# Kernel optimization log

Measured on AMD Instinct MI355X. Metric: run time of the kernel, lower is better.

Reference implementation:

```python
import jax, jax.numpy as jnp
import numpy as np

D_MODEL = 1024
D_FF = 4 * D_MODEL
NUM_EXPERTS = 8
TOP_K = 2
TOKENS = 4096


def setup_inputs() -> dict:
    key = jax.random.key(0)
    ks = jax.random.split(key, 8)
    s = 0.02
    x = jax.random.normal(ks[0], (TOKENS, D_MODEL), dtype=jnp.float32)
    Wg = jax.random.normal(ks[1], (D_MODEL, NUM_EXPERTS), dtype=jnp.float32) * s
    bg = jnp.zeros((NUM_EXPERTS,), dtype=jnp.float32)
    W1 = jax.random.normal(ks[2], (NUM_EXPERTS, D_MODEL, D_FF), dtype=jnp.float32) * s
    b1 = jnp.zeros((NUM_EXPERTS, D_FF), dtype=jnp.float32)
    W2 = jax.random.normal(ks[3], (NUM_EXPERTS, D_FF, D_MODEL), dtype=jnp.float32) * s
    b2 = jnp.zeros((NUM_EXPERTS, D_MODEL), dtype=jnp.float32)
    return {"x": x, "Wg": Wg, "bg": bg, "W1": W1, "b1": b1, "W2": W2, "b2": b2}


def reference(x, Wg, bg, W1, b1, W2, b2):
    # Gating: softmax over experts, select top-k indices per token.
    gate_scores = jax.nn.softmax(x @ Wg + bg, axis=-1)        # [T, E]
    _, top_k_idx = jax.lax.top_k(gate_scores, TOP_K)          # [T, K]
    # Binary combine mask: 1 where expert selected (top_k indices are distinct).
    # NOTE: original sums selected expert outputs WITHOUT gate weighting.
    mask = jnp.sum(jax.nn.one_hot(top_k_idx, NUM_EXPERTS, dtype=x.dtype), axis=1)  # [T, E]
    out = jnp.zeros_like(x)
    for e in range(NUM_EXPERTS):  # small fixed expert count
        h = jax.nn.relu(x @ W1[e] + b1[e])                    # [T, 4D]
        y = h @ W2[e] + b2[e]                                 # [T, D]
        out = out + mask[:, e:e + 1] * y
    return out
```

## Files before the change

kernel.cpp:

```cpp
#include <hip/hip_runtime.h>
#include <hip/hip_bf16.h>

#define T_TOKENS 4096
#define DM 1024
#define DF 4096
#define NE 8
#define MAXROWS 9216

typedef float f32x4 __attribute__((ext_vector_type(4)));
typedef short bf16x8 __attribute__((ext_vector_type(8)));

__device__ __forceinline__ unsigned short f2bf(float f) {
    union { float f; unsigned int u; } v; v.f = f;
    unsigned int r = v.u + 0x7fffu + ((v.u >> 16) & 1u);
    return (unsigned short)(r >> 16);
}

__device__ __forceinline__ void g2l16(const void* g, void* l) {
    __builtin_amdgcn_global_load_lds(
        (const __attribute__((address_space(1))) void*)g,
        (__attribute__((address_space(3))) void*)l, 16, 0, 0);
}

__global__ __launch_bounds__(256) void gate_kernel(
    const float* __restrict__ x, const float* __restrict__ Wg, const float* __restrict__ bg,
    int* __restrict__ counts, int* __restrict__ topk)
{
    int wave = threadIdx.x >> 6;
    int lane = threadIdx.x & 63;
    int t = blockIdx.x * 4 + wave;
    float acc[NE];
#pragma unroll
    for (int e = 0; e < NE; e++) acc[e] = 0.f;
    const float* xr = x + (size_t)t * DM;
#pragma unroll
    for (int i = 0; i < DM / 64; i++) {
        int d = lane + i * 64;
        float xv = xr[d];
        const float4* wg = (const float4*)(Wg + d * NE);
        float4 w0 = wg[0], w1 = wg[1];
        acc[0] += xv * w0.x; acc[1] += xv * w0.y; acc[2] += xv * w0.z; acc[3] += xv * w0.w;
        acc[4] += xv * w1.x; acc[5] += xv * w1.y; acc[6] += xv * w1.z; acc[7] += xv * w1.w;
    }
#pragma unroll
    for (int e = 0; e < NE; e++) {
#pragma unroll
        for (int off = 32; off > 0; off >>= 1)
            acc[e] += __shfl_down(acc[e], off);
    }
    if (lane == 0) {
        float lg[NE];
#pragma unroll
        for (int e = 0; e < NE; e++) lg[e] = acc[e] + bg[e];
        int b1i = 0; float b1v = lg[0];
        for (int e = 1; e < NE; e++) if (lg[e] > b1v) { b1v = lg[e]; b1i = e; }
        int b2i = -1; float b2v = -1e30f;
        for (int e = 0; e < NE; e++) {
            if (e == b1i) continue;
            if (b2i < 0 || lg[e] > b2v) { b2v = lg[e]; b2i = e; }
        }
        topk[t * 2 + 0] = b1i;
        topk[t * 2 + 1] = b2i;
        atomicAdd(&counts[b1i], 1);
        atomicAdd(&counts[b2i], 1);
    }
}

__global__ __launch_bounds__(256) void scatter_kernel(
    const int* __restrict__ counts, const int* __restrict__ topk,
    int* __restrict__ offsets, int* __restrict__ list)
{
    __shared__ int offs[NE + 1];
    __shared__ int cur[NE];
    if (threadIdx.x == 0) {
        int s = 0;
        for (int e = 0; e < NE; e++) {
            offs[e] = s; offsets[e] = s;
            s += (counts[e] + 127) & ~127;
        }
        offs[NE] = s; offsets[NE] = s;
    }
    if (threadIdx.x < NE) cur[threadIdx.x] = 0;
    __syncthreads();
    for (int i = threadIdx.x; i < T_TOKENS * 2; i += 256) {
        int e = topk[i];
        int pos = atomicAdd(&cur[e], 1);
        list[offs[e] + pos] = i >> 1;
    }
    __syncthreads();
    for (int e = 0; e < NE; e++) {
        int s = offs[e] + counts[e];
        int t = offs[e + 1];
        for (int i = s + threadIdx.x; i < t; i += 256) list[i] = -1;
    }
}

__global__ __launch_bounds__(256) void cvt_x_kernel(
    const float* __restrict__ x, unsigned short* __restrict__ xb)
{
    int i = (blockIdx.x * 256 + threadIdx.x) * 4;
    float4 v = *(const float4*)(x + i);
    unsigned short o[4] = { f2bf(v.x), f2bf(v.y), f2bf(v.z), f2bf(v.w) };
    *(uint2*)(xb + i) = *(const uint2*)o;
}

__global__ __launch_bounds__(256) void tr_cvt_kernel(
    const float* __restrict__ src, unsigned short* __restrict__ dst, int K, int N)
{
    const int e = blockIdx.z;
    src += (size_t)e * K * N;
    dst += (size_t)e * N * K;
    const int n0 = blockIdx.x * 64, k0 = blockIdx.y * 64;
    __shared__ unsigned short tile[64][68];
    const int t = threadIdx.x;
    const int tx = t & 63, ty = t >> 6;
#pragma unroll
    for (int r = 0; r < 16; r++) {
        int k = ty * 16 + r;
        tile[tx][k] = f2bf(src[(size_t)(k0 + k) * N + n0 + tx]);
    }
    __syncthreads();
    const int kx = (t & 15) * 4, ny = t >> 4;
#pragma unroll
    for (int r = 0; r < 4; r++) {
        int n = ny + r * 16;
        *(uint2*)(dst + (size_t)(n0 + n) * K + k0 + kx) = *(const uint2*)&tile[n][kx];
    }
}

__global__ __launch_bounds__(256) void gemm1_kernel(
    const unsigned short* __restrict__ xb, const unsigned short* __restrict__ W1T,
    const float* __restrict__ b1, const int* __restrict__ offsets,
    const int* __restrict__ list, unsigned short* __restrict__ H)
{
    const int total = offsets[NE];
    const int row0 = blockIdx.x * 128;
    if (row0 >= total) return;
    int e = 0;
    while (row0 >= offsets[e + 1]) e++;
    const int n0 = blockIdx.y * 128;

    __shared__ unsigned short Asm[2][4096];
    __shared__ unsigned short Bsm[2][4096];

    const int tid = threadIdx.x;
    const int w = tid >> 6, lane = tid & 63;
    const int quad = lane >> 4, l16 = lane & 15;
    const int wm = w >> 1, wn = w & 1;

    const int sr = lane >> 2;
    const int sc = (((lane & 3) ^ ((sr >> 1) & 3))) * 8;
    const int qx8 = (quad ^ ((l16 >> 1) & 3)) * 8;

    const int ra1 = 32 * w + sr, ra2 = ra1 + 16;
    int t1 = list[row0 + ra1]; if (t1 < 0) t1 = 0;
    int t2 = list[row0 + ra2]; if (t2 < 0) t2 = 0;
    const unsigned short* gA1 = xb + (size_t)t1 * DM + sc;
    const unsigned short* gA2 = xb + (size_t)t2 * DM + sc;
    const unsigned short* Wb = W1T + (size_t)e * DF * DM;
    const unsigned short* gB1 = Wb + (size_t)(n0 + 32 * w + sr) * DM + sc;
    const unsigned short* gB2 = gB1 + (size_t)16 * DM;
    unsigned short* lA1 = &Asm[0][(2 * w) * 512];
    unsigned short* lA2 = &Asm[0][(2 * w + 1) * 512];
    unsigned short* lB1 = &Bsm[0][(2 * w) * 512];
    unsigned short* lB2 = &Bsm[0][(2 * w + 1) * 512];

    f32x4 acc[4][4];
#pragma unroll
    for (int i = 0; i < 4; i++)
#pragma unroll
        for (int j = 0; j < 4; j++) acc[i][j] = (f32x4){0.f, 0.f, 0.f, 0.f};

#define STAGE1(b, kk) do { \
        g2l16(gA1 + (kk), lA1 + (b) * 4096); \
        g2l16(gA2 + (kk), lA2 + (b) * 4096); \
        g2l16(gB1 + (kk), lB1 + (b) * 4096); \
        g2l16(gB2 + (kk), lB2 + (b) * 4096); } while (0)

    STAGE1(0, 0);
    __syncthreads();
#pragma unroll 2
    for (int kk = 0; kk < DM; kk += 32) {
        const int b = (kk >> 5) & 1;
        if (kk + 32 < DM) STAGE1(b ^ 1, kk + 32);
        bf16x8 af[4];
#pragma unroll
        for (int i = 0; i < 4; i++)
            af[i] = *(const bf16x8*)&Asm[b][(wm * 64 + i * 16 + l16) * 32 + qx8];
#pragma unroll
        for (int j = 0; j < 4; j++) {
            bf16x8 bfv = *(const bf16x8*)&Bsm[b][(wn * 64 + j * 16 + l16) * 32 + qx8];
#pragma unroll
            for (int i = 0; i < 4; i++)
                acc[i][j] = __builtin_amdgcn_mfma_f32_16x16x32_bf16(af[i], bfv, acc[i][j], 0, 0, 0);
        }
        __syncthreads();
    }
#undef STAGE1

    const float* bias = b1 + e * DF;
#pragma unroll
    for (int j = 0; j < 4; j++) {
        int n = n0 + wn * 64 + j * 16 + l16;
        float bj = bias[n];
#pragma unroll
        for (int i = 0; i < 4; i++) {
            int row = row0 + wm * 64 + i * 16 + quad * 4;
#pragma unroll
            for (int r = 0; r < 4; r++) {
                float v = acc[i][j][r] + bj;
                v = fmaxf(v, 0.f);
                H[(size_t)(row + r) * DF + n] = f2bf(v);
            }
        }
    }
}

__global__ __launch_bounds__(256) void gemm2_kernel(
    const unsigned short* __restrict__ H, const unsigned short* __restrict__ W2T,
    const float* __restrict__ b2, const int* __restrict__ offsets,
    const int* __restrict__ list, float* __restrict__ out)
{
    const int total = offsets[NE];
    const int row0 = blockIdx.x * 128;
    if (row0 >= total) return;
    int e = 0;
    while (row0 >= offsets[e + 1]) e++;
    const int n0 = blockIdx.y * 128;
    const int kz = blockIdx.z;
    const int k0 = kz * (DF / 2);

    __shared__ unsigned short Asm[2][4096];
    __shared__ unsigned short Bsm[2][4096];

    const int tid = threadIdx.x;
    const int w = tid >> 6, lane = tid & 63;
    const int quad = lane >> 4, l16 = lane & 15;
    const int wm = w >> 1, wn = w & 1;

    const int sr = lane >> 2;
    const int sc = (((lane & 3) ^ ((sr >> 1) & 3))) * 8;
    const int qx8 = (quad ^ ((l16 >> 1) & 3)) * 8;

    const unsigned short* gA1 = H + (size_t)(row0 + 32 * w + sr) * DF + k0 + sc;
    const unsigned short* gA2 = gA1 + (size_t)16 * DF;
    const unsigned short* Wb = W2T + (size_t)e * DM * DF;
    const unsigned short* gB1 = Wb + (size_t)(n0 + 32 * w + sr) * DF + k0 + sc;
    const unsigned short* gB2 = gB1 + (size_t)16 * DF;
    unsigned short* lA1 = &Asm[0][(2 * w) * 512];
    unsigned short* lA2 = &Asm[0][(2 * w + 1) * 512];
    unsigned short* lB1 = &Bsm[0][(2 * w) * 512];
    unsigned short* lB2 = &Bsm[0][(2 * w + 1) * 512];

    f32x4 acc[4][4];
#pragma unroll
    for (int i = 0; i < 4; i++)
#pragma unroll
        for (int j = 0; j < 4; j++) acc[i][j] = (f32x4){0.f, 0.f, 0.f, 0.f};

#define STAGE2(b, kk) do { \
        g2l16(gA1 + (kk), lA1 + (b) * 4096); \
        g2l16(gA2 + (kk), lA2 + (b) * 4096); \
        g2l16(gB1 + (kk), lB1 + (b) * 4096); \
        g2l16(gB2 + (kk), lB2 + (b) * 4096); } while (0)

    STAGE2(0, 0);
    __syncthreads();
#pragma unroll 2
    for (int kk = 0; kk < DF / 2; kk += 32) {
        const int b = (kk >> 5) & 1;
        if (kk + 32 < DF / 2) STAGE2(b ^ 1, kk + 32);
        bf16x8 af[4];
#pragma unroll
        for (int i = 0; i < 4; i++)
            af[i] = *(const bf16x8*)&Asm[b][(wm * 64 + i * 16 + l16) * 32 + qx8];
#pragma unroll
        for (int j = 0; j < 4; j++) {
            bf16x8 bfv = *(const bf16x8*)&Bsm[b][(wn * 64 + j * 16 + l16) * 32 + qx8];
#pragma unroll
            for (int i = 0; i < 4; i++)
                acc[i][j] = __builtin_amdgcn_mfma_f32_16x16x32_bf16(af[i], bfv, acc[i][j], 0, 0, 0);
        }
        __syncthreads();
    }
#undef STAGE2

    const float* bias = b2 + e * DM;
#pragma unroll
    for (int j = 0; j < 4; j++) {
        int n = n0 + wn * 64 + j * 16 + l16;
        float bj = (kz == 0) ? bias[n] : 0.f;
#pragma unroll
        for (int i = 0; i < 4; i++) {
            int row = row0 + wm * 64 + i * 16 + quad * 4;
#pragma unroll
            for (int r = 0; r < 4; r++) {
                int tk = list[row + r];
                if (tk >= 0)
                    atomicAdd(&out[(size_t)tk * DM + n], acc[i][j][r] + bj);
            }
        }
    }
}

extern "C" void kernel_launch(void* const* d_in, const int* in_sizes, int n_in,
                              void* d_out, int out_size, void* d_ws, size_t ws_size,
                              hipStream_t stream)
{
    const float* x  = (const float*)d_in[0];
    const float* Wg = (const float*)d_in[1];
    const float* bg = (const float*)d_in[2];
    const float* W1 = (const float*)d_in[3];
    const float* b1 = (const float*)d_in[4];
    const float* W2 = (const float*)d_in[5];
    const float* b2 = (const float*)d_in[6];
    float* out = (float*)d_out;

    char* ws = (char*)d_ws;
    int* counts  = (int*)(ws + 0);
    int* offsets = (int*)(ws + 64);
    int* topk    = (int*)(ws + 256);
    int* list    = (int*)(ws + 33024);
    unsigned short* xb = (unsigned short*)(ws + (1u << 20));
    unsigned short* WT = (unsigned short*)(ws + (16u << 20));
    unsigned short* Hb = (unsigned short*)(ws + (80u << 20));

    hipMemsetAsync(counts, 0, NE * sizeof(int), stream);
    hipMemsetAsync(d_out, 0, (size_t)out_size * sizeof(float), stream);

    gate_kernel<<<T_TOKENS / 4, 256, 0, stream>>>(x, Wg, bg, counts, topk);
    scatter_kernel<<<1, 256, 0, stream>>>(counts, topk, offsets, list);
    cvt_x_kernel<<<T_TOKENS * DM / 1024, 256, 0, stream>>>(x, xb);

    tr_cvt_kernel<<<dim3(DF / 64, DM / 64, NE), 256, 0, stream>>>(W1, WT, DM, DF);
    gemm1_kernel<<<dim3(MAXROWS / 128, DF / 128), 256, 0, stream>>>(
        xb, WT, b1, offsets, list, Hb);

    tr_cvt_kernel<<<dim3(DM / 64, DF / 64, NE), 256, 0, stream>>>(W2, WT, DF, DM);
    gemm2_kernel<<<dim3(MAXROWS / 128, DM / 128, 2), 256, 0, stream>>>(
        Hb, WT, b2, offsets, list, out);
}
```

Baseline: 716.2 us.

## Triple-buffer LDS pipeline with vmcnt waits; drop split-K in gemm2

Both expert GEMMs move from double-buffered LDS staging with a full __syncthreads per k-step to a three-stage ring. Loads run two tiles ahead, and an explicit s_waitcnt vmcnt(4) plus a raw s_barrier is used in place of draining all outstanding loads. The aim is to hide global-to-LDS latency better. gemm2 also drops its 2-way split-K over DF, which halves the atomicAdd traffic to the output but also halves the grid size and doubles the K loop per block.

```diff
diff --git a/kernel.cpp b/kernel.cpp
--- a/kernel.cpp
+++ b/kernel.cpp
@@ -140,8 +140,8 @@
     while (row0 >= offsets[e + 1]) e++;
     const int n0 = blockIdx.y * 128;
 
-    __shared__ unsigned short Asm[2][4096];
-    __shared__ unsigned short Bsm[2][4096];
+    __shared__ unsigned short Asm[3][4096];
+    __shared__ unsigned short Bsm[3][4096];
 
     const int tid = threadIdx.x;
     const int w = tid >> 6, lane = tid & 63;
@@ -177,12 +177,7 @@
         g2l16(gB1 + (kk), lB1 + (b) * 4096); \
         g2l16(gB2 + (kk), lB2 + (b) * 4096); } while (0)
 
-    STAGE1(0, 0);
-    __syncthreads();
-#pragma unroll 2
-    for (int kk = 0; kk < DM; kk += 32) {
-        const int b = (kk >> 5) & 1;
-        if (kk + 32 < DM) STAGE1(b ^ 1, kk + 32);
+    auto compute = [&](int b) {
         bf16x8 af[4];
 #pragma unroll
         for (int i = 0; i < 4; i++)
@@ -194,8 +189,24 @@
             for (int i = 0; i < 4; i++)
                 acc[i][j] = __builtin_amdgcn_mfma_f32_16x16x32_bf16(af[i], bfv, acc[i][j], 0, 0, 0);
         }
-        __syncthreads();
-    }
+    };
+
+    const int NT = DM / 32;
+    STAGE1(0, 0);
+    STAGE1(1, 32);
+    int bc = 0, bs = 2;
+    for (int t = 0; t < NT - 1; ++t) {
+        asm volatile("s_waitcnt vmcnt(4)" ::: "memory");
+        __builtin_amdgcn_s_barrier();
+        __builtin_amdgcn_sched_barrier(0);
+        if (t + 2 < NT) STAGE1(bs, (t + 2) * 32);
+        compute(bc);
+        bc = (bc == 2) ? 0 : bc + 1;
+        bs = (bs == 2) ? 0 : bs + 1;
+    }
+    asm volatile("s_waitcnt vmcnt(0)" ::: "memory");
+    __builtin_amdgcn_s_barrier();
+    compute(bc);
 #undef STAGE1
 
     const float* bias = b1 + e * DF;
@@ -227,11 +238,9 @@
     int e = 0;
     while (row0 >= offsets[e + 1]) e++;
     const int n0 = blockIdx.y * 128;
-    const int kz = blockIdx.z;
-    const int k0 = kz * (DF / 2);
-
-    __shared__ unsigned short Asm[2][4096];
-    __shared__ unsigned short Bsm[2][4096];
+
+    __shared__ unsigned short Asm[3][4096];
+    __shared__ unsigned short Bsm[3][4096];
 
     const int tid = threadIdx.x;
     const int w = tid >> 6, lane = tid & 63;
@@ -242,10 +251,10 @@
     const int sc = (((lane & 3) ^ ((sr >> 1) & 3))) * 8;
     const int qx8 = (quad ^ ((l16 >> 1) & 3)) * 8;
 
-    const unsigned short* gA1 = H + (size_t)(row0 + 32 * w + sr) * DF + k0 + sc;
+    const unsigned short* gA1 = H + (size_t)(row0 + 32 * w + sr) * DF + sc;
     const unsigned short* gA2 = gA1 + (size_t)16 * DF;
     const unsigned short* Wb = W2T + (size_t)e * DM * DF;
-    const unsigned short* gB1 = Wb + (size_t)(n0 + 32 * w + sr) * DF + k0 + sc;
+    const unsigned short* gB1 = Wb + (size_t)(n0 + 32 * w + sr) * DF + sc;
     const unsigned short* gB2 = gB1 + (size_t)16 * DF;
     unsigned short* lA1 = &Asm[0][(2 * w) * 512];
     unsigned short* lA2 = &Asm[0][(2 * w + 1) * 512];
@@ -264,12 +273,7 @@
         g2l16(gB1 + (kk), lB1 + (b) * 4096); \
         g2l16(gB2 + (kk), lB2 + (b) * 4096); } while (0)
 
-    STAGE2(0, 0);
-    __syncthreads();
-#pragma unroll 2
-    for (int kk = 0; kk < DF / 2; kk += 32) {
-        const int b = (kk >> 5) & 1;
-        if (kk + 32 < DF / 2) STAGE2(b ^ 1, kk + 32);
+    auto compute = [&](int b) {
         bf16x8 af[4];
 #pragma unroll
         for (int i = 0; i < 4; i++)
@@ -281,15 +285,31 @@
             for (int i = 0; i < 4; i++)
                 acc[i][j] = __builtin_amdgcn_mfma_f32_16x16x32_bf16(af[i], bfv, acc[i][j], 0, 0, 0);
         }
-        __syncthreads();
-    }
+    };
+
+    const int NT = DF / 32;
+    STAGE2(0, 0);
+    STAGE2(1, 32);
+    int bc = 0, bs = 2;
+    for (int t = 0; t < NT - 1; ++t) {
+        asm volatile("s_waitcnt vmcnt(4)" ::: "memory");
+        __builtin_amdgcn_s_barrier();
+        __builtin_amdgcn_sched_barrier(0);
+        if (t + 2 < NT) STAGE2(bs, (t + 2) * 32);
+        compute(bc);
+        bc = (bc == 2) ? 0 : bc + 1;
+        bs = (bs == 2) ? 0 : bs + 1;
+    }
+    asm volatile("s_waitcnt vmcnt(0)" ::: "memory");
+    __builtin_amdgcn_s_barrier();
+    compute(bc);
 #undef STAGE2
 
     const float* bias = b2 + e * DM;
 #pragma unroll
     for (int j = 0; j < 4; j++) {
         int n = n0 + wn * 64 + j * 16 + l16;
-        float bj = (kz == 0) ? bias[n] : 0.f;
+        float bj = bias[n];
 #pragma unroll
         for (int i = 0; i < 4; i++) {
             int row = row0 + wm * 64 + i * 16 + quad * 4;
@@ -337,6 +357,6 @@
         xb, WT, b1, offsets, list, Hb);
 
     tr_cvt_kernel<<<dim3(DM / 64, DF / 64, NE), 256, 0, stream>>>(W2, WT, DF, DM);
-    gemm2_kernel<<<dim3(MAXROWS / 128, DM / 128, 2), 256, 0, stream>>>(
+    gemm2_kernel<<<dim3(MAXROWS / 128, DM / 128), 256, 0, stream>>>(
         Hb, WT, b2, offsets, list, out);
 }
```

New measurement: 805.7 us. 12.5% more time.
